# Optimization experiments

Measured on AMD Instinct MI355X. Metric: run time of the kernel, lower is better.

## Reference

```python
import jax, jax.numpy as jnp
import numpy as np

H = 2  # attention heads (n_heads)


def _time_enc(t, tw, tb):
    # TGN TimeEncode: cos(t * w + b); t [...,] -> [..., T]
    return jnp.cos(t[..., None] * tw + tb)


def _level0(nodes, node_features, memory_tab):
    # memory[src] + node_features[src]
    return memory_tab[nodes] + node_features[nodes]


def _aggregate(l, src_feat, src_te, neigh, ete, efeat, mask,
               Wq, bq, Wk, bk, Wv, bv, Wo, bo, fc1_w, fc1_b, fc2_w, fc2_b):
    # Temporal graph attention (TGN TemporalAttentionLayer) with padding mask.
    N, K, _ = neigh.shape
    Dq = Wq.shape[-1]
    dh = Dq // H
    q_in = jnp.concatenate([src_feat[:, None, :], src_te], axis=-1)   # [N,1,Dq]
    k_in = jnp.concatenate([neigh, ete, efeat], axis=-1)              # [N,K,Dk]
    q = (q_in @ Wq[l] + bq[l]).reshape(N, 1, H, dh)
    k = (k_in @ Wk[l] + bk[l]).reshape(N, K, H, dh)
    v = (k_in @ Wv[l] + bv[l]).reshape(N, K, H, dh)
    scores = jnp.einsum('nqhd,nkhd->nhqk', q, k) / jnp.sqrt(jnp.asarray(dh, q.dtype))
    all_masked = mask.all(axis=-1)                                    # [N]
    # TGN trick: un-mask column 0 for fully-masked rows, zero output later
    eff_mask = mask & ~(all_masked[:, None] & (jnp.arange(K) == 0))
    scores = jnp.where(eff_mask[:, None, None, :], -1e9, scores)
    attn = jax.nn.softmax(scores, axis=-1)
    o = jnp.einsum('nhqk,nkhd->nqhd', attn, v).reshape(N, Dq)
    o = o @ Wo[l] + bo[l]
    o = jnp.where(all_masked[:, None], 0.0, o)
    # MergeLayer: fc2(relu(fc1(cat[attn_out, src_feat])))
    h = jax.nn.relu(jnp.concatenate([o, src_feat], axis=-1) @ fc1_w[l] + fc1_b[l])
    return h @ fc2_w[l] + fc2_b[l]


def setup_inputs() -> dict:
    key = jax.random.key(0)
    ks = jax.random.split(key, 24)
    B, K, Nn, Ne, D, T = 2048, 20, 1_000_000, 1_000_000, 128, 128
    Dq, Dk = D + T, D + T + D
    inp = {}
    inp['node_features'] = jax.random.normal(ks[0], (Nn, D), jnp.float32) * 0.1
    inp['edge_feat_table'] = jax.random.normal(ks[1], (Ne, D), jnp.float32) * 0.1
    inp['memory_tab'] = jax.random.normal(ks[2], (Nn, D), jnp.float32) * 0.1
    inp['timestamps'] = jax.random.uniform(ks[3], (B,), jnp.float32) * 100.0
    inp['etimes_src'] = jax.random.uniform(ks[4], (B, K), jnp.float32) * 100.0
    inp['etimes_nbr'] = jax.random.uniform(ks[5], (B * K, K), jnp.float32) * 100.0
    inp['tw'] = jax.random.normal(ks[6], (T,), jnp.float32)
    inp['tb'] = jax.random.normal(ks[7], (T,), jnp.float32)
    inp['Wq'] = jax.random.normal(ks[8], (2, Dq, Dq), jnp.float32) / np.sqrt(Dq)
    inp['bq'] = jnp.zeros((2, Dq), jnp.float32)
    inp['Wk'] = jax.random.normal(ks[9], (2, Dk, Dq), jnp.float32) / np.sqrt(Dk)
    inp['bk'] = jnp.zeros((2, Dq), jnp.float32)
    inp['Wv'] = jax.random.normal(ks[10], (2, Dk, Dq), jnp.float32) / np.sqrt(Dk)
    inp['bv'] = jnp.zeros((2, Dq), jnp.float32)
    inp['Wo'] = jax.random.normal(ks[11], (2, Dq, Dq), jnp.float32) / np.sqrt(Dq)
    inp['bo'] = jnp.zeros((2, Dq), jnp.float32)
    inp['fc1_w'] = jax.random.normal(ks[12], (2, Dq + D, D), jnp.float32) / np.sqrt(Dq + D)
    inp['fc1_b'] = jnp.zeros((2, D), jnp.float32)
    inp['fc2_w'] = jax.random.normal(ks[13], (2, D, D), jnp.float32) / np.sqrt(D)
    inp['fc2_b'] = jnp.zeros((2, D), jnp.float32)
    inp['source_nodes'] = jax.random.randint(ks[14], (B,), 0, Nn)
    inp['nbrs_src'] = jax.random.randint(ks[15], (B, K), 0, Nn)
    inp['eidx_src'] = jax.random.randint(ks[16], (B, K), 0, Ne)
    inp['nbrs_nbr'] = jax.random.randint(ks[17], (B * K, K), 0, Nn)
    inp['eidx_nbr'] = jax.random.randint(ks[18], (B * K, K), 0, Ne)
    return inp


def reference(node_features, edge_feat_table, memory_tab, timestamps,
              etimes_src, etimes_nbr, tw, tb,
              Wq, bq, Wk, bk, Wv, bv, Wo, bo, fc1_w, fc1_b, fc2_w, fc2_b,
              source_nodes, nbrs_src, eidx_src, nbrs_nbr, eidx_nbr):
    B, K = nbrs_src.shape
    D = node_features.shape[-1]
    params = (Wq, bq, Wk, bk, Wv, bv, Wo, bo, fc1_w, fc1_b, fc2_w, fc2_b)

    def layer1(nodes, ts, nbrs, eidx, etimes):
        # one temporal-attention hop (n_layers == 1 recursion level)
        src = _level0(nodes, node_features, memory_tab)                 # [N,D]
        neigh = _level0(nbrs.reshape(-1), node_features, memory_tab).reshape(*nbrs.shape, D)
        ete = _time_enc(ts[:, None] - etimes, tw, tb)                   # [N,K,T]
        src_te = _time_enc(jnp.zeros((nodes.shape[0], 1), ts.dtype), tw, tb)
        efeat = edge_feat_table[eidx]                                   # [N,K,De]
        mask = nbrs == 0
        return _aggregate(0, src, src_te, neigh, ete, efeat, mask, *params)

    # layer-1 embedding of sources (recursion uses same temporal neighbors)
    src_conv = layer1(source_nodes, timestamps, nbrs_src, eidx_src, etimes_src)  # [B,D]
    # layer-1 embedding of the sources' neighbors
    ts_rep = jnp.repeat(timestamps, K)                                  # [B*K]
    neigh_emb = layer1(nbrs_src.reshape(-1), ts_rep, nbrs_nbr, eidx_nbr, etimes_nbr)
    neigh_emb = neigh_emb.reshape(B, K, D)
    # layer-2 aggregation over the sources' neighbors
    ete = _time_enc(timestamps[:, None] - etimes_src, tw, tb)           # [B,K,T]
    src_te = _time_enc(jnp.zeros((B, 1), timestamps.dtype), tw, tb)
    efeat = edge_feat_table[eidx_src]
    mask = nbrs_src == 0
    return _aggregate(1, src_conv, src_te, neigh_emb, ete, efeat, mask, *params)
```

## Files before the change

kernel.cpp:

```cpp
#include <hip/hip_runtime.h>
#include <hip/hip_bf16.h>

#define NB   2048
#define KN   20
#define DF   128
#define DQ   256
#define DKI  384
#define NR1  43008
#define SCALE 0.08838834764831845f

typedef short s16x8 __attribute__((ext_vector_type(8)));
typedef short s16x4 __attribute__((ext_vector_type(4)));
typedef float f32x4 __attribute__((ext_vector_type(4)));

__device__ __hip_bfloat16 g_S   [(size_t)NR1*256];
__device__ __hip_bfloat16 g_QKH [(size_t)NR1*768];
__device__ __hip_bfloat16 g_CTX [(size_t)NR1*768];
__device__ __hip_bfloat16 g_Ob  [(size_t)NR1*256];
__device__ __hip_bfloat16 g_FC1A[(size_t)NR1*384];
__device__ __hip_bfloat16 g_Hb  [(size_t)NR1*128];
__device__ float          g_out1[(size_t)NR1*DF];
__device__ float          g_Wqk [2*256*768];
__device__ float          g_bqk [2*768];
__device__ unsigned char  g_allm[NR1];
__device__ __hip_bfloat16 g_Bqk[2*196608];
__device__ __hip_bfloat16 g_Bv [4*49152];
__device__ __hip_bfloat16 g_Bo [2*65536];
__device__ __hip_bfloat16 g_B1 [2*49152];
__device__ __hip_bfloat16 g_B2 [2*16384];

__device__ __forceinline__ short f2bf(float v) {
  union { __hip_bfloat16 h; short s; } u; u.h = __float2bfloat16(v); return u.s;
}
__device__ __forceinline__ float2 bfpair(unsigned u) {
  union { unsigned u2; float f; } a, b;
  a.u2 = u << 16;
  b.u2 = u & 0xFFFF0000u;
  float2 r; r.x = a.f; r.y = b.f; return r;
}
__device__ __forceinline__ s16x4 pack4(float x, float y, float z, float w) {
  s16x4 o; o[0]=f2bf(x); o[1]=f2bf(y); o[2]=f2bf(z); o[3]=f2bf(w); return o;
}
__device__ __forceinline__ unsigned packbf2(float2 v) {
  return (unsigned)(unsigned short)f2bf(v.x) | ((unsigned)(unsigned short)f2bf(v.y) << 16);
}

__global__ __launch_bounds__(256)
void k_wqk(const float* __restrict__ Wq, const float* __restrict__ Wk,
           const float* __restrict__ bq) {
  int idx = blockIdx.x*256 + threadIdx.x;
  int L = idx / 196608, rem = idx % 196608;
  int n = rem >> 8, co = rem & 255;
  int h = n / 384, i = n - h*384;
  const float* wqp = Wq + (size_t)L*DQ*DQ  + (size_t)co*DQ + h*128;
  const float* wkp = Wk + (size_t)L*DKI*DQ + (size_t)i*DQ  + h*128;
  float acc = 0.f;
  #pragma unroll 4
  for (int c = 0; c < 128; ++c) acc += wqp[c]*wkp[c];
  g_Wqk[(size_t)(L*256 + co)*768 + n] = acc;
  if (co == 0) {
    const float* bqp = bq + L*DQ + h*128;
    float b = 0.f;
    for (int c = 0; c < 128; ++c) b += bqp[c]*wkp[c];
    g_bqk[L*768 + n] = b;
  }
}

__global__ __launch_bounds__(256)
void k_btile(const float* __restrict__ src, int ldsrc, int K, int N,
             __hip_bfloat16* __restrict__ dst) {
  int slot = blockIdx.x*256 + threadIdx.x;
  if (slot >= (K*N)/8) return;
  int cl = slot & 15, t = slot >> 4;
  int kgn = K >> 3;
  int kg = t % kgn, nt = t / kgn;
  int n = nt*16 + cl;
  s16x8 o;
  #pragma unroll
  for (int e = 0; e < 8; ++e) o[e] = f2bf(src[(size_t)(kg*8 + e)*ldsrc + n]);
  *(s16x8*)(dst + (size_t)slot*8) = o;
}

template<int L>
__global__ __launch_bounds__(256)
void k_prep(const float* __restrict__ nf, const float* __restrict__ mem,
            const float* __restrict__ tb,
            const int* __restrict__ srcn, const int* __restrict__ nbs) {
  const int tid = threadIdx.x;
  const int rl = tid >> 5, q = tid & 31, d0 = q*4;
  const int r = blockIdx.x*8 + rl;
  float ax, ay, az, aw;
  if (L == 0) {
    int node = (r < NB) ? srcn[r] : nbs[r - NB];
    float4 x = *(const float4*)(mem + (size_t)node*DF + d0);
    float4 y = *(const float4*)(nf  + (size_t)node*DF + d0);
    ax=x.x+y.x; ay=x.y+y.y; az=x.z+y.z; aw=x.w+y.w;
  } else {
    float4 x = *(const float4*)(g_out1 + (size_t)r*DF + d0);
    ax=x.x; ay=x.y; az=x.z; aw=x.w;
  }
  *(s16x4*)(g_S + (size_t)r*256 + d0) = pack4(ax, ay, az, aw);
  *(s16x4*)(g_S + (size_t)r*256 + 128 + d0) =
      pack4(cosf(tb[d0]), cosf(tb[d0+1]), cosf(tb[d0+2]), cosf(tb[d0+3]));
  *(s16x4*)(g_FC1A + (size_t)r*384 + 256 + d0) = pack4(ax, ay, az, aw);
}

template<int L>
__global__ __launch_bounds__(256, 4)
void k_edge(const float* __restrict__ nf, const float* __restrict__ ef,
            const float* __restrict__ mem, const float* __restrict__ tsv,
            const float* __restrict__ ets, const float* __restrict__ etn,
            const float* __restrict__ tw,  const float* __restrict__ tb,
            const int* __restrict__ nbs, const int* __restrict__ eis,
            const int* __restrict__ nbn, const int* __restrict__ ein,
            const __hip_bfloat16* __restrict__ QKH,
            __hip_bfloat16* __restrict__ CTX)
{
  const int tid = threadIdx.x;
  const int lane = tid & 63, w = tid >> 6;
  const int r = blockIdx.x*4 + w;

  int raw_ = 1, nd_ = 0, ei_ = 0; float dt_ = 0.f;
  if (lane < KN) {
    if (L == 0) {
      if (r < NB) { raw_ = nbs[r*KN+lane]; nd_ = raw_; ei_ = eis[r*KN+lane]; dt_ = tsv[r] - ets[r*KN+lane]; }
      else { int mm = (r-NB)*KN + lane; raw_ = nbn[mm]; nd_ = raw_; ei_ = ein[mm]; dt_ = tsv[(r-NB)/KN] - etn[mm]; }
    } else {
      raw_ = nbs[r*KN+lane]; nd_ = NB + r*KN + lane; ei_ = eis[r*KN+lane]; dt_ = tsv[r] - ets[r*KN+lane];
    }
  }
  unsigned long long bal = __ballot(lane < KN && raw_ == 0);
  unsigned mb = (unsigned)(bal & 0xFFFFFull);
  if (lane == 0) g_allm[r] = (mb == 0xFFFFFu) ? 1 : 0;

  const __hip_bfloat16* Qr = QKH + (size_t)r*768;
  float2 q0[3], q1[3];
  #pragma unroll
  for (int seg = 0; seg < 3; ++seg) {
    q0[seg] = bfpair(*(const unsigned*)(Qr +       seg*128 + 2*lane));
    q1[seg] = bfpair(*(const unsigned*)(Qr + 384 + seg*128 + 2*lane));
  }
  float2 twr = *(const float2*)(tw + 2*lane);
  float2 tbr = *(const float2*)(tb + 2*lane);

  float m0 = -3.0e38f, m1 = -3.0e38f;
  float su0 = 0.f, su1 = 0.f;
  float2 c0n = {0,0}, c0t = {0,0}, c0e = {0,0};
  float2 c1n = {0,0}, c1t = {0,0}, c1e = {0,0};

  #pragma unroll
  for (int c0i = 0; c0i < KN; c0i += 5) {
    int nds[5], eir[5]; float dtr[5];
    #pragma unroll
    for (int e = 0; e < 5; ++e) {
      nds[e] = __shfl(nd_, c0i + e);
      eir[e] = __shfl(ei_, c0i + e);
      dtr[e] = __shfl(dt_, c0i + e);
    }
    float2 vm[5], vf[5], vef[5];
    #pragma unroll
    for (int e = 0; e < 5; ++e) {
      if (L == 0) {
        vm[e] = *(const float2*)(mem + (size_t)nds[e]*DF + 2*lane);
        vf[e] = *(const float2*)(nf  + (size_t)nds[e]*DF + 2*lane);
      } else {
        vm[e] = *(const float2*)(g_out1 + (size_t)nds[e]*DF + 2*lane);
      }
      vef[e] = *(const float2*)(ef + (size_t)eir[e]*DF + 2*lane);
    }
    #pragma unroll
    for (int e = 0; e < 5; ++e) {
      float2 vn;
      if (L == 0) { vn.x = vm[e].x + vf[e].x; vn.y = vm[e].y + vf[e].y; }
      else        vn = vm[e];
      float2 vt;
      vt.x = __cosf(dtr[e]*twr.x + tbr.x);
      vt.y = __cosf(dtr[e]*twr.y + tbr.y);
      float p0 = vn.x*q0[0].x + vn.y*q0[0].y + vt.x*q0[1].x + vt.y*q0[1].y
               + vef[e].x*q0[2].x + vef[e].y*q0[2].y;
      float p1 = vn.x*q1[0].x + vn.y*q1[0].y + vt.x*q1[1].x + vt.y*q1[1].y
               + vef[e].x*q1[2].x + vef[e].y*q1[2].y;
      #pragma unroll
      for (int off = 1; off < 64; off <<= 1) {
        p0 += __shfl_xor(p0, off);
        p1 += __shfl_xor(p1, off);
      }
      const bool msk = (mb >> (c0i + e)) & 1u;
      float s0 = msk ? -1e9f : p0*SCALE;
      float s1 = msk ? -1e9f : p1*SCALE;
      if (s0 > m0) {
        float f = __expf(m0 - s0);
        su0 *= f;
        c0n.x *= f; c0n.y *= f; c0t.x *= f; c0t.y *= f; c0e.x *= f; c0e.y *= f;
        m0 = s0;
      }
      float w0 = __expf(s0 - m0);
      su0 += w0;
      c0n.x += w0*vn.x;    c0n.y += w0*vn.y;
      c0t.x += w0*vt.x;    c0t.y += w0*vt.y;
      c0e.x += w0*vef[e].x; c0e.y += w0*vef[e].y;
      if (s1 > m1) {
        float f = __expf(m1 - s1);
        su1 *= f;
        c1n.x *= f; c1n.y *= f; c1t.x *= f; c1t.y *= f; c1e.x *= f; c1e.y *= f;
        m1 = s1;
      }
      float w1 = __expf(s1 - m1);
      su1 += w1;
      c1n.x += w1*vn.x;    c1n.y += w1*vn.y;
      c1t.x += w1*vt.x;    c1t.y += w1*vt.y;
      c1e.x += w1*vef[e].x; c1e.y += w1*vef[e].y;
    }
  }

  float i0 = 1.f / su0, i1 = 1.f / su1;
  c0n.x *= i0; c0n.y *= i0; c0t.x *= i0; c0t.y *= i0; c0e.x *= i0; c0e.y *= i0;
  c1n.x *= i1; c1n.y *= i1; c1t.x *= i1; c1t.y *= i1; c1e.x *= i1; c1e.y *= i1;
  unsigned* C32 = (unsigned*)(CTX + (size_t)r*768);
  C32[0*64 + lane] = packbf2(c0n);
  C32[1*64 + lane] = packbf2(c0t);
  C32[2*64 + lane] = packbf2(c0e);
  C32[3*64 + lane] = packbf2(c1n);
  C32[4*64 + lane] = packbf2(c1t);
  C32[5*64 + lane] = packbf2(c1e);
}

template<int KT, bool F32OUT, bool RELU, bool MASK>
__global__ __launch_bounds__(256, 2)
void k_gemm(const __hip_bfloat16* __restrict__ A, int lda,
            const __hip_bfloat16* __restrict__ B, int kgtot, int nblk,
            void* __restrict__ Cout, int ldc,
            const float* __restrict__ bias,
            const unsigned char* __restrict__ mask)
{
  __shared__ __hip_bfloat16 As[2][128*40];
  __shared__ __hip_bfloat16 Bs[2][128*32];
  const int tid  = threadIdx.x;
  const int lane = tid & 63, wid = tid >> 6;
  const int wm = wid >> 1, wn = wid & 1;
  const int rl = lane & 15, kgs = lane >> 4;
  const int bm = blockIdx.x / nblk, bn = blockIdx.x % nblk;

  f32x4 acc[4][4];
  #pragma unroll
  for (int i = 0; i < 4; ++i)
    #pragma unroll
    for (int j = 0; j < 4; ++j) acc[i][j] = (f32x4){0.f,0.f,0.f,0.f};

  #define STAGE(T, BUF) {                                                      \
    _Pragma("unroll")                                                          \
    for (int i_ = 0; i_ < 2; ++i_) {                                           \
      int row_ = i_*64 + (tid >> 2), kc_ = (tid & 3)*8;                        \
      s16x8 v_ = *(const s16x8*)(A + (size_t)(bm*128 + row_)*lda + (T)*32 + kc_); \
      *(s16x8*)(&As[BUF][row_*40 + kc_]) = v_;                                 \
    }                                                                          \
    _Pragma("unroll")                                                          \
    for (int i_ = 0; i_ < 2; ++i_) {                                           \
      int slot_ = i_*256 + tid;                                                \
      int nt_ = slot_ >> 6, kg_ = (slot_ >> 4) & 3, cl_ = slot_ & 15;          \
      s16x8 w_ = *(const s16x8*)(B + ((size_t)(bn*8 + nt_)*kgtot + (T)*4 + kg_)*128 + cl_*8); \
      *(s16x8*)(&Bs[BUF][slot_*8]) = w_;                                       \
    } }

  STAGE(0, 0);
  __syncthreads();
  int buf = 0;
  for (int t = 0; t < KT; ++t) {
    if (t < KT-1) STAGE(t+1, buf ^ 1);
    s16x8 af[4], bfm[4];
    #pragma unroll
    for (int mtl = 0; mtl < 4; ++mtl)
      af[mtl] = *(const s16x8*)(&As[buf][(wm*64 + mtl*16 + rl)*40 + kgs*8]);
    #pragma unroll
    for (int ntl = 0; ntl < 4; ++ntl)
      bfm[ntl] = *(const s16x8*)(&Bs[buf][((wn*4 + ntl)*4 + kgs)*128 + rl*8]);
    #pragma unroll
    for (int mtl = 0; mtl < 4; ++mtl)
      #pragma unroll
      for (int ntl = 0; ntl < 4; ++ntl)
        acc[mtl][ntl] = __builtin_amdgcn_mfma_f32_16x16x32_bf16(af[mtl], bfm[ntl], acc[mtl][ntl], 0, 0, 0);
    __syncthreads();
    buf ^= 1;
  }
  #undef STAGE

  #pragma unroll
  for (int mtl = 0; mtl < 4; ++mtl) {
    #pragma unroll
    for (int ntl = 0; ntl < 4; ++ntl) {
      int gcol = bn*128 + wn*64 + ntl*16 + rl;
      float bb = bias ? bias[gcol] : 0.f;
      #pragma unroll
      for (int rg = 0; rg < 4; ++rg) {
        int grow = bm*128 + wm*64 + mtl*16 + kgs*4 + rg;
        float v = acc[mtl][ntl][rg] + bb;
        if (RELU) v = fmaxf(v, 0.f);
        if (MASK) { if (mask[grow]) v = 0.f; }
        if (F32OUT) ((float*)Cout)[(size_t)grow*ldc + gcol] = v;
        else ((__hip_bfloat16*)Cout)[(size_t)grow*ldc + gcol] = __float2bfloat16(v);
      }
    }
  }
}

extern "C" void kernel_launch(void* const* d_in, const int* in_sizes, int n_in,
                              void* d_out, int out_size, void* d_ws, size_t ws_size,
                              hipStream_t stream) {
  (void)in_sizes; (void)n_in; (void)out_size; (void)ws_size; (void)d_ws;
  const float* nf   = (const float*)d_in[0];
  const float* ef   = (const float*)d_in[1];
  const float* mem  = (const float*)d_in[2];
  const float* tsv  = (const float*)d_in[3];
  const float* ets  = (const float*)d_in[4];
  const float* etn  = (const float*)d_in[5];
  const float* tw   = (const float*)d_in[6];
  const float* tb   = (const float*)d_in[7];
  const float* Wq   = (const float*)d_in[8];
  const float* bq   = (const float*)d_in[9];
  const float* Wk   = (const float*)d_in[10];
  const float* bv   = (const float*)d_in[13];
  const float* Wv   = (const float*)d_in[12];
  const float* Wo   = (const float*)d_in[14];
  const float* bo   = (const float*)d_in[15];
  const float* f1w  = (const float*)d_in[16];
  const float* f1b  = (const float*)d_in[17];
  const float* f2w  = (const float*)d_in[18];
  const float* f2b  = (const float*)d_in[19];
  const int* srcn   = (const int*)d_in[20];
  const int* nbs    = (const int*)d_in[21];
  const int* eis    = (const int*)d_in[22];
  const int* nbn    = (const int*)d_in[23];
  const int* ein    = (const int*)d_in[24];
  float* out = (float*)d_out;

  __hip_bfloat16 *S, *QKH, *CTX, *Ob, *FC1A, *Hb, *Bqk, *Bv, *Bo, *B1, *B2;
  float *Wqkf, *bqkf, *out1f;
  unsigned char* allm;
  hipGetSymbolAddress((void**)&S,    HIP_SYMBOL(g_S));
  hipGetSymbolAddress((void**)&QKH,  HIP_SYMBOL(g_QKH));
  hipGetSymbolAddress((void**)&CTX,  HIP_SYMBOL(g_CTX));
  hipGetSymbolAddress((void**)&Ob,   HIP_SYMBOL(g_Ob));
  hipGetSymbolAddress((void**)&FC1A, HIP_SYMBOL(g_FC1A));
  hipGetSymbolAddress((void**)&Hb,   HIP_SYMBOL(g_Hb));
  hipGetSymbolAddress((void**)&Bqk,  HIP_SYMBOL(g_Bqk));
  hipGetSymbolAddress((void**)&Bv,   HIP_SYMBOL(g_Bv));
  hipGetSymbolAddress((void**)&Bo,   HIP_SYMBOL(g_Bo));
  hipGetSymbolAddress((void**)&B1,   HIP_SYMBOL(g_B1));
  hipGetSymbolAddress((void**)&B2,   HIP_SYMBOL(g_B2));
  hipGetSymbolAddress((void**)&Wqkf, HIP_SYMBOL(g_Wqk));
  hipGetSymbolAddress((void**)&bqkf, HIP_SYMBOL(g_bqk));
  hipGetSymbolAddress((void**)&out1f,HIP_SYMBOL(g_out1));
  hipGetSymbolAddress((void**)&allm, HIP_SYMBOL(g_allm));

  hipLaunchKernelGGL(k_wqk, dim3(1536), dim3(256), 0, stream, Wq, Wk, bq);
  for (int L = 0; L < 2; ++L) {
    hipLaunchKernelGGL(k_btile, dim3(96), dim3(256), 0, stream, Wqkf + (size_t)L*256*768, 768, 256, 768, Bqk + (size_t)L*196608);
    for (int h = 0; h < 2; ++h)
      hipLaunchKernelGGL(k_btile, dim3(24), dim3(256), 0, stream, Wv + (size_t)L*DKI*DQ + h*128, 256, 384, 128, Bv + (size_t)(L*2+h)*49152);
    hipLaunchKernelGGL(k_btile, dim3(32), dim3(256), 0, stream, Wo + (size_t)L*DQ*DQ,    256, 256, 256, Bo + (size_t)L*65536);
    hipLaunchKernelGGL(k_btile, dim3(24), dim3(256), 0, stream, f1w + (size_t)L*384*128, 128, 384, 128, B1 + (size_t)L*49152);
    hipLaunchKernelGGL(k_btile, dim3(8),  dim3(256), 0, stream, f2w + (size_t)L*128*128, 128, 128, 128, B2 + (size_t)L*16384);
  }

  {
    const int R = NR1, BMg = R/128;
    hipLaunchKernelGGL((k_prep<0>), dim3(R/8), dim3(256), 0, stream, nf, mem, tb, srcn, nbs);
    hipLaunchKernelGGL((k_gemm<8,false,false,false>), dim3(BMg*6), dim3(256), 0, stream,
        S, 256, Bqk, 32, 6, QKH, 768, bqkf, (const unsigned char*)nullptr);
    hipLaunchKernelGGL((k_edge<0>), dim3(R/4), dim3(256), 0, stream,
        nf, ef, mem, tsv, ets, etn, tw, tb, nbs, eis, nbn, ein, QKH, CTX);
    for (int h = 0; h < 2; ++h)
      hipLaunchKernelGGL((k_gemm<12,false,false,false>), dim3(BMg), dim3(256), 0, stream,
          CTX + h*384, 768, Bv + (size_t)h*49152, 48, 1, Ob + h*128, 256, bv + h*128, (const unsigned char*)nullptr);
    hipLaunchKernelGGL((k_gemm<8,false,false,true>), dim3(BMg*2), dim3(256), 0, stream,
        Ob, 256, Bo, 32, 2, FC1A, 384, bo, allm);
    hipLaunchKernelGGL((k_gemm<12,false,true,false>), dim3(BMg), dim3(256), 0, stream,
        FC1A, 384, B1, 48, 1, Hb, 128, f1b, (const unsigned char*)nullptr);
    hipLaunchKernelGGL((k_gemm<4,true,false,false>), dim3(BMg), dim3(256), 0, stream,
        Hb, 128, B2, 16, 1, out1f, 128, f2b, (const unsigned char*)nullptr);
  }
  {
    const int R = NB, BMg = R/128;
    hipLaunchKernelGGL((k_prep<1>), dim3(R/8), dim3(256), 0, stream, nf, mem, tb, srcn, nbs);
    hipLaunchKernelGGL((k_gemm<8,false,false,false>), dim3(BMg*6), dim3(256), 0, stream,
        S, 256, Bqk + 196608, 32, 6, QKH, 768, bqkf + 768, (const unsigned char*)nullptr);
    hipLaunchKernelGGL((k_edge<1>), dim3(R/4), dim3(256), 0, stream,
        nf, ef, mem, tsv, ets, etn, tw, tb, nbs, eis, nbn, ein, QKH, CTX);
    for (int h = 0; h < 2; ++h)
      hipLaunchKernelGGL((k_gemm<12,false,false,false>), dim3(BMg), dim3(256), 0, stream,
          CTX + h*384, 768, Bv + (size_t)(2+h)*49152, 48, 1, Ob + h*128, 256, bv + 256 + h*128, (const unsigned char*)nullptr);
    hipLaunchKernelGGL((k_gemm<8,false,false,true>), dim3(BMg*2), dim3(256), 0, stream,
        Ob, 256, Bo + 65536, 32, 2, FC1A, 384, bo + 256, allm);
    hipLaunchKernelGGL((k_gemm<12,false,true,false>), dim3(BMg), dim3(256), 0, stream,
        FC1A, 384, B1 + 49152, 48, 1, Hb, 128, f1b + 128, (const unsigned char*)nullptr);
    hipLaunchKernelGGL((k_gemm<4,true,false,false>), dim3(BMg), dim3(256), 0, stream,
        Hb, 128, B2 + 16384, 16, 1, out, 128, f2b + 128, (const unsigned char*)nullptr);
  }
}
```

Baseline: 612.6 us.

## Fold constant time-encoding into QK bias, fuse MLP GEMMs and batch weight prep

```diff
diff --git a/kernel.cpp b/kernel.cpp
--- a/kernel.cpp
+++ b/kernel.cpp
@@ -13,17 +13,17 @@
 typedef short s16x4 __attribute__((ext_vector_type(4)));
 typedef float f32x4 __attribute__((ext_vector_type(4)));
 
-__device__ __hip_bfloat16 g_S   [(size_t)NR1*256];
+__device__ __hip_bfloat16 g_S   [(size_t)NR1*128];
 __device__ __hip_bfloat16 g_QKH [(size_t)NR1*768];
 __device__ __hip_bfloat16 g_CTX [(size_t)NR1*768];
 __device__ __hip_bfloat16 g_Ob  [(size_t)NR1*256];
 __device__ __hip_bfloat16 g_FC1A[(size_t)NR1*384];
-__device__ __hip_bfloat16 g_Hb  [(size_t)NR1*128];
 __device__ float          g_out1[(size_t)NR1*DF];
 __device__ float          g_Wqk [2*256*768];
 __device__ float          g_bqk [2*768];
+__device__ float          g_bqkv[2*768];
 __device__ unsigned char  g_allm[NR1];
-__device__ __hip_bfloat16 g_Bqk[2*196608];
+__device__ __hip_bfloat16 g_Bqk[2*98304];
 __device__ __hip_bfloat16 g_Bv [4*49152];
 __device__ __hip_bfloat16 g_Bo [2*65536];
 __device__ __hip_bfloat16 g_B1 [2*49152];
@@ -46,30 +46,45 @@
 }
 
 __global__ __launch_bounds__(256)
-void k_wqk(const float* __restrict__ Wq, const float* __restrict__ Wk,
-           const float* __restrict__ bq) {
-  int idx = blockIdx.x*256 + threadIdx.x;
-  int L = idx / 196608, rem = idx % 196608;
-  int n = rem >> 8, co = rem & 255;
-  int h = n / 384, i = n - h*384;
-  const float* wqp = Wq + (size_t)L*DQ*DQ  + (size_t)co*DQ + h*128;
-  const float* wkp = Wk + (size_t)L*DKI*DQ + (size_t)i*DQ  + h*128;
-  float acc = 0.f;
-  #pragma unroll 4
-  for (int c = 0; c < 128; ++c) acc += wqp[c]*wkp[c];
-  g_Wqk[(size_t)(L*256 + co)*768 + n] = acc;
-  if (co == 0) {
-    const float* bqp = bq + L*DQ + h*128;
-    float b = 0.f;
-    for (int c = 0; c < 128; ++c) b += bqp[c]*wkp[c];
-    g_bqk[L*768 + n] = b;
-  }
-}
-
-__global__ __launch_bounds__(256)
-void k_btile(const float* __restrict__ src, int ldsrc, int K, int N,
-             __hip_bfloat16* __restrict__ dst) {
-  int slot = blockIdx.x*256 + threadIdx.x;
+void k_wprep1(const float* __restrict__ Wq, const float* __restrict__ Wk,
+              const float* __restrict__ bq, const float* __restrict__ Wv,
+              const float* __restrict__ Wo, const float* __restrict__ f1w,
+              const float* __restrict__ f2w) {
+  int b = blockIdx.x;
+  if (b < 1536) {
+    int idx = b*256 + threadIdx.x;
+    int L = idx / 196608, rem = idx % 196608;
+    int n = rem >> 8, co = rem & 255;
+    int h = n / 384, i = n - h*384;
+    const float* wqp = Wq + (size_t)L*DQ*DQ  + (size_t)co*DQ + h*128;
+    const float* wkp = Wk + (size_t)L*DKI*DQ + (size_t)i*DQ  + h*128;
+    float acc = 0.f;
+    #pragma unroll 4
+    for (int c = 0; c < 128; ++c) acc += wqp[c]*wkp[c];
+    g_Wqk[(size_t)(L*256 + co)*768 + n] = acc;
+    if (co == 0) {
+      const float* bqp = bq + L*DQ + h*128;
+      float bb = 0.f;
+      for (int c = 0; c < 128; ++c) bb += bqp[c]*wkp[c];
+      g_bqk[L*768 + n] = bb;
+    }
+    return;
+  }
+  b -= 1536;
+  const float* src; int ldsrc, K, N; __hip_bfloat16* dst;
+  if (b < 96)       { int j = b/24; int L=j>>1, h=j&1;
+                      src = Wv + (size_t)L*DKI*DQ + h*128; ldsrc=256; K=384; N=128;
+                      dst = g_Bv + (size_t)j*49152; b %= 24; }
+  else if (b < 160) { b -= 96; int L = b/32;
+                      src = Wo + (size_t)L*DQ*DQ; ldsrc=256; K=256; N=256;
+                      dst = g_Bo + (size_t)L*65536; b %= 32; }
+  else if (b < 208) { b -= 160; int L = b/24;
+                      src = f1w + (size_t)L*384*128; ldsrc=128; K=384; N=128;
+                      dst = g_B1 + (size_t)L*49152; b %= 24; }
+  else              { b -= 208; int L = b/8;
+                      src = f2w + (size_t)L*128*128; ldsrc=128; K=128; N=128;
+                      dst = g_B2 + (size_t)L*16384; b %= 8; }
+  int slot = b*256 + threadIdx.x;
   if (slot >= (K*N)/8) return;
   int cl = slot & 15, t = slot >> 4;
   int kgn = K >> 3;
@@ -81,10 +96,33 @@
   *(s16x8*)(dst + (size_t)slot*8) = o;
 }
 
+__global__ __launch_bounds__(256)
+void k_wprep2(const float* __restrict__ tb) {
+  int b = blockIdx.x;
+  if (b < 96) {
+    int L = b / 48;
+    int slot = (b % 48)*256 + threadIdx.x;
+    int cl = slot & 15, t = slot >> 4;
+    int kg = t & 15, nt = t >> 4;
+    int n = nt*16 + cl;
+    s16x8 o;
+    #pragma unroll
+    for (int e = 0; e < 8; ++e)
+      o[e] = f2bf(g_Wqk[(size_t)(L*256 + kg*8 + e)*768 + n] * SCALE);
+    *(s16x8*)(g_Bqk + (size_t)L*98304 + (size_t)slot*8) = o;
+  } else {
+    int idx = (b - 96)*256 + threadIdx.x;
+    int L = idx / 768, n = idx % 768;
+    float acc = g_bqk[idx];
+    for (int c = 0; c < 128; ++c)
+      acc += cosf(tb[c]) * g_Wqk[(size_t)(L*256 + 128 + c)*768 + n];
+    g_bqkv[idx] = acc * SCALE;
+  }
+}
+
 template<int L>
 __global__ __launch_bounds__(256)
 void k_prep(const float* __restrict__ nf, const float* __restrict__ mem,
-            const float* __restrict__ tb,
             const int* __restrict__ srcn, const int* __restrict__ nbs) {
   const int tid = threadIdx.x;
   const int rl = tid >> 5, q = tid & 31, d0 = q*4;
@@ -99,10 +137,9 @@
     float4 x = *(const float4*)(g_out1 + (size_t)r*DF + d0);
     ax=x.x; ay=x.y; az=x.z; aw=x.w;
   }
-  *(s16x4*)(g_S + (size_t)r*256 + d0) = pack4(ax, ay, az, aw);
-  *(s16x4*)(g_S + (size_t)r*256 + 128 + d0) =
-      pack4(cosf(tb[d0]), cosf(tb[d0+1]), cosf(tb[d0+2]), cosf(tb[d0+3]));
-  *(s16x4*)(g_FC1A + (size_t)r*384 + 256 + d0) = pack4(ax, ay, az, aw);
+  s16x4 p = pack4(ax, ay, az, aw);
+  *(s16x4*)(g_S + (size_t)r*128 + d0) = p;
+  *(s16x4*)(g_FC1A + (size_t)r*384 + 256 + d0) = p;
 }
 
 template<int L>
@@ -186,8 +223,8 @@
         p1 += __shfl_xor(p1, off);
       }
       const bool msk = (mb >> (c0i + e)) & 1u;
-      float s0 = msk ? -1e9f : p0*SCALE;
-      float s1 = msk ? -1e9f : p1*SCALE;
+      float s0 = msk ? -1e9f : p0;
+      float s1 = msk ? -1e9f : p1;
       if (s0 > m0) {
         float f = __expf(m0 - s0);
         su0 *= f;
@@ -231,7 +268,7 @@
             const __hip_bfloat16* __restrict__ B, int kgtot, int nblk,
             void* __restrict__ Cout, int ldc,
             const float* __restrict__ bias,
-            const unsigned char* __restrict__ mask)
+            const unsigned char* __restrict__ mask, int acolbn)
 {
   __shared__ __hip_bfloat16 As[2][128*40];
   __shared__ __hip_bfloat16 Bs[2][128*32];
@@ -251,7 +288,7 @@
     _Pragma("unroll")                                                          \
     for (int i_ = 0; i_ < 2; ++i_) {                                           \
       int row_ = i_*64 + (tid >> 2), kc_ = (tid & 3)*8;                        \
-      s16x8 v_ = *(const s16x8*)(A + (size_t)(bm*128 + row_)*lda + (T)*32 + kc_); \
+      s16x8 v_ = *(const s16x8*)(A + (size_t)(bm*128 + row_)*lda + bn*acolbn + (T)*32 + kc_); \
       *(s16x8*)(&As[BUF][row_*40 + kc_]) = v_;                                 \
     }                                                                          \
     _Pragma("unroll")                                                          \
@@ -298,6 +335,133 @@
         if (MASK) { if (mask[grow]) v = 0.f; }
         if (F32OUT) ((float*)Cout)[(size_t)grow*ldc + gcol] = v;
         else ((__hip_bfloat16*)Cout)[(size_t)grow*ldc + gcol] = __float2bfloat16(v);
+      }
+    }
+  }
+}
+
+__global__ __launch_bounds__(256, 2)
+void k_mlp(const __hip_bfloat16* __restrict__ A,
+           const __hip_bfloat16* __restrict__ B1t,
+           const __hip_bfloat16* __restrict__ B2t,
+           const float* __restrict__ b1, const float* __restrict__ b2,
+           float* __restrict__ Cout)
+{
+  __shared__ __hip_bfloat16 As[2][128*40];
+  __shared__ __hip_bfloat16 Bs[2][128*32];
+  __shared__ __hip_bfloat16 Hb[128*136];
+  const int tid  = threadIdx.x;
+  const int lane = tid & 63, wid = tid >> 6;
+  const int wm = wid >> 1, wn = wid & 1;
+  const int rl = lane & 15, kgs = lane >> 4;
+  const int bm = blockIdx.x;
+
+  f32x4 acc[4][4];
+  #pragma unroll
+  for (int i = 0; i < 4; ++i)
+    #pragma unroll
+    for (int j = 0; j < 4; ++j) acc[i][j] = (f32x4){0.f,0.f,0.f,0.f};
+
+  #define STAGE1(T, BUF) {                                                     \
+    _Pragma("unroll")                                                          \
+    for (int i_ = 0; i_ < 2; ++i_) {                                           \
+      int row_ = i_*64 + (tid >> 2), kc_ = (tid & 3)*8;                        \
+      s16x8 v_ = *(const s16x8*)(A + (size_t)(bm*128 + row_)*384 + (T)*32 + kc_); \
+      *(s16x8*)(&As[BUF][row_*40 + kc_]) = v_;                                 \
+    }                                                                          \
+    _Pragma("unroll")                                                          \
+    for (int i_ = 0; i_ < 2; ++i_) {                                           \
+      int slot_ = i_*256 + tid;                                                \
+      int nt_ = slot_ >> 6, kg_ = (slot_ >> 4) & 3, cl_ = slot_ & 15;          \
+      s16x8 w_ = *(const s16x8*)(B1t + ((size_t)nt_*48 + (T)*4 + kg_)*128 + cl_*8); \
+      *(s16x8*)(&Bs[BUF][slot_*8]) = w_;                                       \
+    } }
+
+  STAGE1(0, 0);
+  __syncthreads();
+  int buf = 0;
+  for (int t = 0; t < 12; ++t) {
+    if (t < 11) STAGE1(t+1, buf ^ 1);
+    s16x8 af[4], bfm[4];
+    #pragma unroll
+    for (int mtl = 0; mtl < 4; ++mtl)
+      af[mtl] = *(const s16x8*)(&As[buf][(wm*64 + mtl*16 + rl)*40 + kgs*8]);
+    #pragma unroll
+    for (int ntl = 0; ntl < 4; ++ntl)
+      bfm[ntl] = *(const s16x8*)(&Bs[buf][((wn*4 + ntl)*4 + kgs)*128 + rl*8]);
+    #pragma unroll
+    for (int mtl = 0; mtl < 4; ++mtl)
+      #pragma unroll
+      for (int ntl = 0; ntl < 4; ++ntl)
+        acc[mtl][ntl] = __builtin_amdgcn_mfma_f32_16x16x32_bf16(af[mtl], bfm[ntl], acc[mtl][ntl], 0, 0, 0);
+    __syncthreads();
+    buf ^= 1;
+  }
+  #undef STAGE1
+
+  #pragma unroll
+  for (int mtl = 0; mtl < 4; ++mtl) {
+    #pragma unroll
+    for (int ntl = 0; ntl < 4; ++ntl) {
+      int col = wn*64 + ntl*16 + rl;
+      float bb = b1[col];
+      #pragma unroll
+      for (int rg = 0; rg < 4; ++rg) {
+        int row = wm*64 + mtl*16 + kgs*4 + rg;
+        union { __hip_bfloat16 h; short s; } u;
+        u.s = f2bf(fmaxf(acc[mtl][ntl][rg] + bb, 0.f));
+        Hb[row*136 + col] = u.h;
+      }
+    }
+  }
+
+  f32x4 acc2[4][4];
+  #pragma unroll
+  for (int i = 0; i < 4; ++i)
+    #pragma unroll
+    for (int j = 0; j < 4; ++j) acc2[i][j] = (f32x4){0.f,0.f,0.f,0.f};
+
+  #define STAGE2(T, BUF) {                                                     \
+    _Pragma("unroll")                                                          \
+    for (int i_ = 0; i_ < 2; ++i_) {                                           \
+      int slot_ = i_*256 + tid;                                                \
+      int nt_ = slot_ >> 6, kg_ = (slot_ >> 4) & 3, cl_ = slot_ & 15;          \
+      s16x8 w_ = *(const s16x8*)(B2t + ((size_t)nt_*16 + (T)*4 + kg_)*128 + cl_*8); \
+      *(s16x8*)(&Bs[BUF][slot_*8]) = w_;                                       \
+    } }
+
+  STAGE2(0, 0);
+  __syncthreads();
+  buf = 0;
+  for (int t = 0; t < 4; ++t) {
+    if (t < 3) STAGE2(t+1, buf ^ 1);
+    s16x8 af[4], bfm[4];
+    #pragma unroll
+    for (int mtl = 0; mtl < 4; ++mtl)
+      af[mtl] = *(const s16x8*)(&Hb[(wm*64 + mtl*16 + rl)*136 + t*32 + kgs*8]);
+    #pragma unroll
+    for (int ntl = 0; ntl < 4; ++ntl)
+      bfm[ntl] = *(const s16x8*)(&Bs[buf][((wn*4 + ntl)*4 + kgs)*128 + rl*8]);
+    #pragma unroll
+    for (int mtl = 0; mtl < 4; ++mtl)
+      #pragma unroll
+      for (int ntl = 0; ntl < 4; ++ntl)
+        acc2[mtl][ntl] = __builtin_amdgcn_mfma_f32_16x16x32_bf16(af[mtl], bfm[ntl], acc2[mtl][ntl], 0, 0, 0);
+    __syncthreads();
+    buf ^= 1;
+  }
+  #undef STAGE2
+
+  #pragma unroll
+  for (int mtl = 0; mtl < 4; ++mtl) {
+    #pragma unroll
+    for (int ntl = 0; ntl < 4; ++ntl) {
+      int gcol = wn*64 + ntl*16 + rl;
+      float bb = b2[gcol];
+      #pragma unroll
+      for (int rg = 0; rg < 4; ++rg) {
+        int grow = bm*128 + wm*64 + mtl*16 + kgs*4 + rg;
+        Cout[(size_t)grow*128 + gcol] = acc2[mtl][ntl][rg] + bb;
       }
     }
   }
@@ -333,67 +497,52 @@
   const int* ein    = (const int*)d_in[24];
   float* out = (float*)d_out;
 
-  __hip_bfloat16 *S, *QKH, *CTX, *Ob, *FC1A, *Hb, *Bqk, *Bv, *Bo, *B1, *B2;
-  float *Wqkf, *bqkf, *out1f;
+  __hip_bfloat16 *S, *QKH, *CTX, *Ob, *FC1A, *Bqk, *Bv, *Bo, *B1, *B2;
+  float *bqkv, *out1f;
   unsigned char* allm;
   hipGetSymbolAddress((void**)&S,    HIP_SYMBOL(g_S));
   hipGetSymbolAddress((void**)&QKH,  HIP_SYMBOL(g_QKH));
   hipGetSymbolAddress((void**)&CTX,  HIP_SYMBOL(g_CTX));
   hipGetSymbolAddress((void**)&Ob,   HIP_SYMBOL(g_Ob));
   hipGetSymbolAddress((void**)&FC1A, HIP_SYMBOL(g_FC1A));
-  hipGetSymbolAddress((void**)&Hb,   HIP_SYMBOL(g_Hb));
   hipGetSymbolAddress((void**)&Bqk,  HIP_SYMBOL(g_Bqk));
   hipGetSymbolAddress((void**)&Bv,   HIP_SYMBOL(g_Bv));
   hipGetSymbolAddress((void**)&Bo,   HIP_SYMBOL(g_Bo));
   hipGetSymbolAddress((void**)&B1,   HIP_SYMBOL(g_B1));
   hipGetSymbolAddress((void**)&B2,   HIP_SYMBOL(g_B2));
-  hipGetSymbolAddress((void**)&Wqkf, HIP_SYMBOL(g_Wqk));
-  hipGetSymbolAddress((void**)&bqkf, HIP_SYMBOL(g_bqk));
+  hipGetSymbolAddress((void**)&bqkv, HIP_SYMBOL(g_bqkv));
   hipGetSymbolAddress((void**)&out1f,HIP_SYMBOL(g_out1));
   hipGetSymbolAddress((void**)&allm, HIP_SYMBOL(g_allm));
 
-  hipLaunchKernelGGL(k_wqk, dim3(1536), dim3(256), 0, stream, Wq, Wk, bq);
-  for (int L = 0; L < 2; ++L) {
-    hipLaunchKernelGGL(k_btile, dim3(96), dim3(256), 0, stream, Wqkf + (size_t)L*256*768, 768, 256, 768, Bqk + (size_t)L*196608);
-    for (int h = 0; h < 2; ++h)
-      hipLaunchKernelGGL(k_btile, dim3(24), dim3(256), 0, stream, Wv + (size_t)L*DKI*DQ + h*128, 256, 384, 128, Bv + (size_t)(L*2+h)*49152);
-    hipLaunchKernelGGL(k_btile, dim3(32), dim3(256), 0, stream, Wo + (size_t)L*DQ*DQ,    256, 256, 256, Bo + (size_t)L*65536);
-    hipLaunchKernelGGL(k_btile, dim3(24), dim3(256), 0, stream, f1w + (size_t)L*384*128, 128, 384, 128, B1 + (size_t)L*49152);
-    hipLaunchKernelGGL(k_btile, dim3(8),  dim3(256), 0, stream, f2w + (size_t)L*128*128, 128, 128, 128, B2 + (size_t)L*16384);
-  }
+  hipLaunchKernelGGL(k_wprep1, dim3(1760), dim3(256), 0, stream, Wq, Wk, bq, Wv, Wo, f1w, f2w);
+  hipLaunchKernelGGL(k_wprep2, dim3(102), dim3(256), 0, stream, tb);
 
   {
     const int R = NR1, BMg = R/128;
-    hipLaunchKernelGGL((k_prep<0>), dim3(R/8), dim3(256), 0, stream, nf, mem, tb, srcn, nbs);
-    hipLaunchKernelGGL((k_gemm<8,false,false,false>), dim3(BMg*6), dim3(256), 0, stream,
-        S, 256, Bqk, 32, 6, QKH, 768, bqkf, (const unsigned char*)nullptr);
+    hipLaunchKernelGGL((k_prep<0>), dim3(R/8), dim3(256), 0, stream, nf, mem, srcn, nbs);
+    hipLaunchKernelGGL((k_gemm<4,false,false,false>), dim3(BMg*6), dim3(256), 0, stream,
+        S, 128, Bqk, 16, 6, QKH, 768, bqkv, (const unsigned char*)nullptr, 0);
     hipLaunchKernelGGL((k_edge<0>), dim3(R/4), dim3(256), 0, stream,
         nf, ef, mem, tsv, ets, etn, tw, tb, nbs, eis, nbn, ein, QKH, CTX);
-    for (int h = 0; h < 2; ++h)
-      hipLaunchKernelGGL((k_gemm<12,false,false,false>), dim3(BMg), dim3(256), 0, stream,
-          CTX + h*384, 768, Bv + (size_t)h*49152, 48, 1, Ob + h*128, 256, bv + h*128, (const unsigned char*)nullptr);
+    hipLaunchKernelGGL((k_gemm<12,false,false,false>), dim3(BMg*2), dim3(256), 0, stream,
+        CTX, 768, Bv, 48, 2, Ob, 256, bv, (const unsigned char*)nullptr, 384);
     hipLaunchKernelGGL((k_gemm<8,false,false,true>), dim3(BMg*2), dim3(256), 0, stream,
-        Ob, 256, Bo, 32, 2, FC1A, 384, bo, allm);
-    hipLaunchKernelGGL((k_gemm<12,false,true,false>), dim3(BMg), dim3(256), 0, stream,
-        FC1A, 384, B1, 48, 1, Hb, 128, f1b, (const unsigned char*)nullptr);
-    hipLaunchKernelGGL((k_gemm<4,true,false,false>), dim3(BMg), dim3(256), 0, stream,
-        Hb, 128, B2, 16, 1, out1f, 128, f2b, (const unsigned char*)nullptr);
+        Ob, 256, Bo, 32, 2, FC1A, 384, bo, allm, 0);
+    hipLaunchKernelGGL(k_mlp, dim3(BMg), dim3(256), 0, stream,
+        FC1A, B1, B2, f1b, f2b, out1f);
   }
   {
     const int R = NB, BMg = R/128;
-    hipLaunchKernelGGL((k_prep<1>), dim3(R/8), dim3(256), 0, stream, nf, mem, tb, srcn, nbs);
-    hipLaunchKernelGGL((k_gemm<8,false,false,false>), dim3(BMg*6), dim3(256), 0, stream,
-        S, 256, Bqk + 196608, 32, 6, QKH, 768, bqkf + 768, (const unsigned char*)nullptr);
+    hipLaunchKernelGGL((k_prep<1>), dim3(R/8), dim3(256), 0, stream, nf, mem, srcn, nbs);
+    hipLaunchKernelGGL((k_gemm<4,false,false,false>), dim3(BMg*6), dim3(256), 0, stream,
+        S, 128, Bqk + 98304, 16, 6, QKH, 768, bqkv + 768, (const unsigned char*)nullptr, 0);
     hipLaunchKernelGGL((k_edge<1>), dim3(R/4), dim3(256), 0, stream,
         nf, ef, mem, tsv, ets, etn, tw, tb, nbs, eis, nbn, ein, QKH, CTX);
-    for (int h = 0; h < 2; ++h)
-      hipLaunchKernelGGL((k_gemm<12,false,false,false>), dim3(BMg), dim3(256), 0, stream,
-          CTX + h*384, 768, Bv + (size_t)(2+h)*49152, 48, 1, Ob + h*128, 256, bv + 256 + h*128, (const unsigned char*)nullptr);
+    hipLaunchKernelGGL((k_gemm<12,false,false,false>), dim3(BMg*2), dim3(256), 0, stream,
+        CTX, 768, Bv + 2*49152, 48, 2, Ob, 256, bv + 256, (const unsigned char*)nullptr, 384);
     hipLaunchKernelGGL((k_gemm<8,false,false,true>), dim3(BMg*2), dim3(256), 0, stream,
-        Ob, 256, Bo + 65536, 32, 2, FC1A, 384, bo + 256, allm);
-    hipLaunchKernelGGL((k_gemm<12,false,true,false>), dim3(BMg), dim3(256), 0, stream,
-        FC1A, 384, B1 + 49152, 48, 1, Hb, 128, f1b + 128, (const unsigned char*)nullptr);
-    hipLaunchKernelGGL((k_gemm<4,true,false,false>), dim3(BMg), dim3(256), 0, stream,
-        Hb, 128, B2 + 16384, 16, 1, out, 128, f2b + 128, (const unsigned char*)nullptr);
-  }
-}
+        Ob, 256, Bo + 65536, 32, 2, FC1A, 384, bo + 256, allm, 0);
+    hipLaunchKernelGGL(k_mlp, dim3(BMg), dim3(256), 0, stream,
+        FC1A, B1 + 49152, B2 + 16384, f1b + 128, f2b + 128, out);
+  }
+}
```

Result: faster. 556.9 us (median of 2 runs) (-9.1%).
